# Kernel tuning notes

Measured on AMD Instinct MI355X. Metric: run time of the kernel, lower is better.

## Reference

```python
import jax, jax.numpy as jnp
import numpy as np

NU, NV, NF = 100000, 50000, 5000
D = 64
S, EUV = 5, 500000
EUF, EVF, EFU, EFV = 1000000, 500000, 1000000, 500000


def _spmm(rows, cols, vals, x, n_out):
    # COO sparse @ dense: out[r] += v * x[c]
    return jax.ops.segment_sum(vals[:, None] * x[cols], rows, num_segments=n_out)


def setup_inputs() -> dict:
    key = jax.random.key(0)
    ks = iter(jax.random.split(key, 32))
    f32 = jnp.float32
    inp = {
        'x_u': jax.random.normal(next(ks), (NU, D), f32),
        'x_v': jax.random.normal(next(ks), (NV, D), f32),
        'x_f': jax.random.normal(next(ks), (NF, D), f32),
    }
    for w in ['W_u_uv', 'W_v_uv', 'W_f2u', 'W_f2v', 'W_u2f', 'W_v2f']:
        inp[w] = jax.random.normal(next(ks), (D, D), f32) * (1.0 / np.sqrt(D))
    def edges(name, shape, n_row, n_col):
        inp[name + '_rows'] = jax.random.randint(next(ks), shape, 0, n_row, jnp.int32)
        inp[name + '_cols'] = jax.random.randint(next(ks), shape, 0, n_col, jnp.int32)
        inp[name + '_vals'] = jax.random.uniform(next(ks), shape, f32)
    edges('uv', (S, EUV), NU, NV)
    edges('vu', (S, EUV), NV, NU)
    edges('uf', (EUF,), NU, NF)
    edges('vf', (EVF,), NV, NF)
    edges('fu', (EFU,), NF, NU)
    edges('fv', (EFV,), NF, NV)
    return inp


def reference(x_u, x_v, x_f, W_u_uv, W_v_uv, W_f2u, W_f2v, W_u2f, W_v2f,
              uv_rows, uv_cols, uv_vals, vu_rows, vu_cols, vu_vals,
              uf_rows, uf_cols, uf_vals, vf_rows, vf_cols, vf_vals,
              fu_rows, fu_cols, fu_vals, fv_rows, fv_cols, fv_vals):
    nu, nv, nf = x_u.shape[0], x_v.shape[0], x_f.shape[0]
    # dense feature transforms (dropout=0 -> identity)
    u2f = x_u @ W_u2f
    v2f = x_v @ W_v2f
    f2u = x_f @ W_f2u
    f2v = x_f @ W_f2v
    tmp_u = x_u @ W_u_uv
    tmp_v = x_v @ W_v_uv
    # sum over rating supports == one segment_sum over flattened edges
    msg_u = _spmm(uv_rows.reshape(-1), uv_cols.reshape(-1), uv_vals.reshape(-1), tmp_v, nu)
    msg_v = _spmm(vu_rows.reshape(-1), vu_cols.reshape(-1), vu_vals.reshape(-1), tmp_u, nv)
    msg_u = msg_u + _spmm(uf_rows, uf_cols, uf_vals, f2u, nu)
    msg_v = msg_v + _spmm(vf_rows, vf_cols, vf_vals, f2v, nv)
    msg_f = _spmm(fu_rows, fu_cols, fu_vals, u2f, nf) + _spmm(fv_rows, fv_cols, fv_vals, v2f, nf)
    return jax.nn.relu(msg_u), jax.nn.relu(msg_v), jax.nn.relu(msg_f)
```

## Files before the change

kernel.cpp:

```cpp
#include <hip/hip_runtime.h>


#define TDIM 64
#define EPB  4096

struct Rel {
    const int* rows; const int* cols; const float* vals;
    int n, chunk0, boff, shift, srcflag, eoff, coladd;
};
struct RelPack { Rel r[6]; };

struct TPack {
    const float* X[3]; const float* W1[3]; const float* W2[3];
    unsigned short* Y1[3]; unsigned short* Y2[3];
    int N[3]; int c0[3];
};

struct FSPack {
    int c0A[3], cntA[3], offA[3];
    int c0B[3], cntB[3], offB[3];
};

struct GatherPack {
    const unsigned* srcA[3]; const unsigned* srcB[3];
    int n0, n1;
};

__device__ __forceinline__ unsigned short f2bf(float f) {
    union { float f; unsigned u; } c; c.f = f;
    unsigned r = c.u + 0x7FFFu + ((c.u >> 16) & 1u);
    return (unsigned short)(r >> 16);
}
__device__ __forceinline__ float bflo(unsigned x) { return __uint_as_float(x << 16); }
__device__ __forceinline__ float bfhi(unsigned x) { return __uint_as_float(x & 0xFFFF0000u); }
__device__ __forceinline__ float pval(unsigned p) {
    return __uint_as_float((p & 0x7FFFu) << 16);
}

__global__ __launch_bounds__(256) void transform_fused_kernel(TPack T)
{
    __shared__ float xsT[64 * 68];
    __shared__ float w1s[64 * 64];
    __shared__ float w2s[64 * 64];

    int t = 0;
    if ((int)blockIdx.x >= T.c0[1]) t = 1;
    if ((int)blockIdx.x >= T.c0[2]) t = 2;
    const float* __restrict__ X  = T.X[t];
    const float* __restrict__ W1 = T.W1[t];
    const float* __restrict__ W2 = T.W2[t];
    unsigned short* __restrict__ Y1 = T.Y1[t];
    unsigned short* __restrict__ Y2 = T.Y2[t];
    const int N    = T.N[t];
    const int row0 = (blockIdx.x - T.c0[t]) * 64;
    const int tid  = threadIdx.x;

    for (int i = tid * 4; i < 4096; i += 256 * 4) {
        *(float4*)&w1s[i] = *(const float4*)&W1[i];
        *(float4*)&w2s[i] = *(const float4*)&W2[i];
    }
    {
        const int r  = tid >> 2;
        const int c0 = (tid & 3) * 16;
        const int gr = row0 + r;
        #pragma unroll
        for (int cc = 0; cc < 16; cc += 4) {
            const int c = c0 + cc;
            float4 v = make_float4(0.f, 0.f, 0.f, 0.f);
            if (gr < N) v = *(const float4*)&X[(size_t)gr * TDIM + c];
            xsT[(c + 0) * 68 + r] = v.x;
            xsT[(c + 1) * 68 + r] = v.y;
            xsT[(c + 2) * 68 + r] = v.z;
            xsT[(c + 3) * 68 + r] = v.w;
        }
    }
    __syncthreads();

    const int tx = tid & 15;
    const int ty = tid >> 4;
    float a1[4][4] = {{0.f}}, a2[4][4] = {{0.f}};

    #pragma unroll 8
    for (int k = 0; k < 64; ++k) {
        const float4 xv = *(const float4*)&xsT[k * 68 + ty * 4];
        const float4 w1 = *(const float4*)&w1s[k * 64 + tx * 4];
        const float4 w2 = *(const float4*)&w2s[k * 64 + tx * 4];
        const float xr[4] = {xv.x, xv.y, xv.z, xv.w};
        const float c1[4] = {w1.x, w1.y, w1.z, w1.w};
        const float c2[4] = {w2.x, w2.y, w2.z, w2.w};
        #pragma unroll
        for (int r = 0; r < 4; ++r)
            #pragma unroll
            for (int c = 0; c < 4; ++c) {
                a1[r][c] = fmaf(xr[r], c1[c], a1[r][c]);
                a2[r][c] = fmaf(xr[r], c2[c], a2[r][c]);
            }
    }
    #pragma unroll
    for (int r = 0; r < 4; ++r) {
        const int gr = row0 + ty * 4 + r;
        if (gr < N) {
            ushort4 o1, o2;
            o1.x = f2bf(a1[r][0]); o1.y = f2bf(a1[r][1]);
            o1.z = f2bf(a1[r][2]); o1.w = f2bf(a1[r][3]);
            o2.x = f2bf(a2[r][0]); o2.y = f2bf(a2[r][1]);
            o2.z = f2bf(a2[r][2]); o2.w = f2bf(a2[r][3]);
            ((ushort4*)Y1)[(size_t)gr * 16 + tx] = o1;
            ((ushort4*)Y2)[(size_t)gr * 16 + tx] = o2;
        }
    }
}

__device__ __forceinline__ int find_rel(const RelPack& P, int chunk) {
    int ri = 0;
    if (chunk >= P.r[1].chunk0) ri = 1;
    if (chunk >= P.r[2].chunk0) ri = 2;
    if (chunk >= P.r[3].chunk0) ri = 3;
    if (chunk >= P.r[4].chunk0) ri = 4;
    if (chunk >= P.r[5].chunk0) ri = 5;
    return ri;
}

__global__ __launch_bounds__(512) void bucketize_cm_kernel(
    RelPack P, unsigned* __restrict__ pay, unsigned char* __restrict__ binb,
    int* __restrict__ localStart, int* __restrict__ bucketTotal, int NB)
{
    __shared__ int cnt[1280];
    __shared__ int sh[512];
    __shared__ unsigned stage_pay[EPB];
    __shared__ unsigned char stage_bin[EPB];

    const int tid   = threadIdx.x;
    const int chunk = blockIdx.x;
    for (int t = tid; t < NB; t += 512) cnt[t] = 0;
    __syncthreads();

    const int ri = find_rel(P, chunk);
    const Rel M = P.r[ri];
    const int i0    = (chunk - M.chunk0) * EPB;
    const int rbase = M.eoff + i0;
    const int count = min(EPB, M.n - i0);

    const int mask = (1 << M.shift) - 1;
    const unsigned sf = (unsigned)M.srcflag;

    int      m_[EPB / 512];
    unsigned x_[EPB / 512];
    #pragma unroll
    for (int k = 0; k < EPB / 512; ++k) {
        const int i = i0 + tid + k * 512;
        m_[k] = -1;
        if (i < M.n) {
            const int row = M.rows[i];
            const int b   = M.boff + (row >> M.shift);
            m_[k] = (b << 8) | (row & mask);
            x_[k] = (unsigned)M.cols[i] + (unsigned)M.coladd;
            atomicAdd(&cnt[b], 1);
        }
    }
    __syncthreads();

    int myv[3]; int lsum = 0;
    #pragma unroll
    for (int j = 0; j < 3; ++j) {
        const int idx = tid * 3 + j;
        myv[j] = (idx < NB) ? cnt[idx] : 0;
        lsum += myv[j];
    }
    sh[tid] = lsum;
    __syncthreads();
    for (int off = 1; off < 512; off <<= 1) {
        const int x = (tid >= off) ? sh[tid - off] : 0;
        __syncthreads();
        sh[tid] += x;
        __syncthreads();
    }
    int prefix = tid ? sh[tid - 1] : 0;
    const size_t lb = (size_t)chunk * (NB + 1);
    #pragma unroll
    for (int j = 0; j < 3; ++j) {
        const int idx = tid * 3 + j;
        if (idx < NB) {
            localStart[lb + idx] = prefix;
            if (myv[j]) atomicAdd(&bucketTotal[idx], myv[j]);
            cnt[idx] = prefix;
        } else if (idx == NB) {
            localStart[lb + NB] = prefix;
        }
        prefix += myv[j];
    }
    __syncthreads();

    #pragma unroll
    for (int k = 0; k < EPB / 512; ++k) {
        if (m_[k] >= 0) {
            const int i   = i0 + tid + k * 512;
            const int b   = m_[k] >> 8;
            const int pos = atomicAdd(&cnt[b], 1);
            stage_pay[pos] = (x_[k] << 15) | ((unsigned)f2bf(M.vals[i]) & 0x7FFFu);
            stage_bin[pos] = (unsigned char)(((m_[k] & 255) << 1) | sf);
        }
    }
    __syncthreads();

    #pragma unroll
    for (int k = 0; k < EPB / 512; ++k) {
        const int j = tid + k * 512;
        if (j < count) pay[rbase + j] = stage_pay[j];
    }
    {
        const int nfull = count >> 2;
        unsigned* bout = (unsigned*)(binb + rbase);
        const unsigned* bsrc = (const unsigned*)stage_bin;
        for (int j = tid; j < nfull; j += 512) bout[j] = bsrc[j];
        if (tid < (count & 3)) binb[rbase + nfull * 4 + tid] = stage_bin[nfull * 4 + tid];
    }
}

__global__ __launch_bounds__(256) void bscan_kernel(
    const int* __restrict__ bucketTotal, int* __restrict__ bbase, int NB)
{
    __shared__ int sh[256];
    __shared__ int carry;
    const int t = threadIdx.x;
    if (t == 0) carry = 0;
    __syncthreads();
    for (int b0 = 0; b0 < NB; b0 += 256) {
        const int idx = b0 + t;
        const int c = (idx < NB) ? bucketTotal[idx] : 0;
        sh[t] = c;
        __syncthreads();
        for (int off = 1; off < 256; off <<= 1) {
            const int x = (t >= off) ? sh[t - off] : 0;
            __syncthreads();
            sh[t] += x;
            __syncthreads();
        }
        const int cbase = carry;
        if (idx < NB) bbase[idx] = cbase + sh[t] - c;
        __syncthreads();
        if (t == 0) carry = cbase + sh[255];
        __syncthreads();
    }
    if (t == 0) bbase[NB] = carry;
}

__global__ __launch_bounds__(512) void finesort_kernel(
    const unsigned* __restrict__ pay, const unsigned char* __restrict__ binb,
    const int* __restrict__ localStart, const int* __restrict__ bbase,
    FSPack F, int* __restrict__ p2, unsigned* __restrict__ arena,
    int nbU, int nbV, int NU, int NV, int NF, int NB, int ntot_rows)
{
    __shared__ int cnt[512];
    __shared__ int sh[512];
    __shared__ int runS[1024], runE[1024];

    const int b   = blockIdx.x;
    const int tid = threadIdx.x;

    int t, lb, rowbase;
    if (b < nbU)              { t = 0; lb = b;              rowbase = 0; }
    else if (b < nbU + nbV)   { t = 1; lb = b - nbU;        rowbase = NU; }
    else                      { t = 2; lb = b - nbU - nbV;  rowbase = NU + NV; }
    const int shift     = (t == 2) ? 6 : 7;
    const int Ntype     = (t == 0) ? NU : (t == 1) ? NV : NF;
    const int row_start = lb << shift;
    const int nrows     = min(1 << shift, Ntype - row_start);
    const int nbins     = (1 << shift) * 2;
    const int grow0     = rowbase + row_start;

    const int nA = F.cntA[t], nB_ = F.cntB[t];
    const int nRuns = nA + nB_;

    for (int i = tid; i < nRuns; i += 512) {
        int c, base;
        if (i < nA) { c = F.c0A[t] + i;        base = F.offA[t] + i * EPB; }
        else        { int k = i - nA;
                      c = F.c0B[t] + k;        base = F.offB[t] + k * EPB; }
        const size_t lbi = (size_t)c * (NB + 1) + b;
        runS[i] = base + localStart[lbi];
        runE[i] = base + localStart[lbi + 1];
    }
    if (tid < nbins) cnt[tid] = 0;
    __syncthreads();

    const int s = bbase[b];
    const int e = bbase[b + 1];
    const int grp = tid >> 4;
    const int gl  = tid & 15;

    for (int ridx = grp; ridx < nRuns; ridx += 32) {
        const int rs = runS[ridx], re = runE[ridx];
        for (int j = rs + gl; j < re; j += 16) {
            atomicAdd(&cnt[binb[j]], 1);
        }
    }
    __syncthreads();

    const int v = (tid < nbins) ? cnt[tid] : 0;
    sh[tid] = v;
    __syncthreads();
    for (int off = 1; off < 512; off <<= 1) {
        const int x = (tid >= off) ? sh[tid - off] : 0;
        __syncthreads();
        sh[tid] += x;
        __syncthreads();
    }
    const int excl = sh[tid] - v;
    if (tid < nbins) cnt[tid] = excl;
    if (tid < nrows * 2) p2[2 * grow0 + tid] = s + excl;
    if (b == NB - 1 && tid == 0) p2[2 * ntot_rows] = e;
    __syncthreads();

    for (int ridx = grp; ridx < nRuns; ridx += 32) {
        const int rs = runS[ridx], re = runE[ridx];
        for (int j = rs + gl; j < re; j += 16) {
            const int bin = binb[j];
            const int pos = s + atomicAdd(&cnt[bin], 1);
            arena[pos] = pay[j];
        }
    }
}

__device__ __forceinline__ void accum_seg(
    const unsigned* __restrict__ src, const unsigned* __restrict__ arena,
    const int s, const int e, const int g, const int li4,
    float (&acc)[8])
{
    if (s >= e) return;
    const int nb = (e - s + 7) >> 3;
    const unsigned* __restrict__ srcp = src + li4;

    unsigned x0[4], x1[4], x2[4], x3[4];
    float w0, w1, w2, w3;

    auto issue = [&](int j, unsigned* x, float& w) {
        const int idx = j + g;
        const bool ok = idx < e;
        const unsigned cv = arena[ok ? idx : s];
        w = ok ? pval(cv) : 0.f;
        const uint4 xv = *(const uint4*)&srcp[(cv >> 15) * 32u];
        x[0] = xv.x; x[1] = xv.y; x[2] = xv.z; x[3] = xv.w;
    };
    auto fmab = [&](const unsigned* x, float w) {
        #pragma unroll
        for (int q = 0; q < 4; ++q) {
            acc[2 * q]     = fmaf(w, bflo(x[q]), acc[2 * q]);
            acc[2 * q + 1] = fmaf(w, bfhi(x[q]), acc[2 * q + 1]);
        }
    };

    issue(s,      x0, w0);
    issue(s + 8,  x1, w1);
    issue(s + 16, x2, w2);
    issue(s + 24, x3, w3);
    __builtin_amdgcn_sched_barrier(0);

    int k = 0;
    for (;;) {
        fmab(x0, w0);
        if (k + 4 < nb) issue(s + (k + 4) * 8, x0, w0);
        __builtin_amdgcn_sched_barrier(0);
        if (++k >= nb) break;
        fmab(x1, w1);
        if (k + 4 < nb) issue(s + (k + 4) * 8, x1, w1);
        __builtin_amdgcn_sched_barrier(0);
        if (++k >= nb) break;
        fmab(x2, w2);
        if (k + 4 < nb) issue(s + (k + 4) * 8, x2, w2);
        __builtin_amdgcn_sched_barrier(0);
        if (++k >= nb) break;
        fmab(x3, w3);
        if (k + 4 < nb) issue(s + (k + 4) * 8, x3, w3);
        __builtin_amdgcn_sched_barrier(0);
        if (++k >= nb) break;
    }
}

__global__ __launch_bounds__(256) void gather_all_kernel(
    const int* __restrict__ p2, const unsigned* __restrict__ arena,
    GatherPack G, float* __restrict__ out, int nrow_total)
{
    const int gid  = (blockIdx.x * 256 + threadIdx.x) >> 6;
    const int lane = threadIdx.x & 63;
    const int g    = lane >> 3;
    const int li   = lane & 7;
    const int li4  = li * 4;
    if (gid >= nrow_total) return;
    const int wid = nrow_total - 1 - gid;

    int seg = 0;
    if (wid >= G.n1)      seg = 2;
    else if (wid >= G.n0) seg = 1;
    seg = __builtin_amdgcn_readfirstlane(seg);

    const int pa = __builtin_amdgcn_readfirstlane(p2[2 * wid]);
    const int pe = __builtin_amdgcn_readfirstlane(p2[2 * wid + 2]);

    float acc[8];
    #pragma unroll
    for (int k = 0; k < 8; ++k) acc[k] = 0.f;

    if (seg < 2) {
        accum_seg(G.srcA[seg], arena, pa, pe, g, li4, acc);
    } else {
        const int pm = __builtin_amdgcn_readfirstlane(p2[2 * wid + 1]);
        accum_seg(G.srcA[2], arena, pa, pm, g, li4, acc);
        accum_seg(G.srcB[2], arena, pm, pe, g, li4, acc);
    }

    #pragma unroll
    for (int k = 0; k < 8; ++k) {
        acc[k] += __shfl_xor(acc[k], 8, 64);
        acc[k] += __shfl_xor(acc[k], 16, 64);
        acc[k] += __shfl_xor(acc[k], 32, 64);
    }

    if (g == 0) {
        float4 o0, o1;
        o0.x = fmaxf(acc[0], 0.f); o0.y = fmaxf(acc[1], 0.f);
        o0.z = fmaxf(acc[2], 0.f); o0.w = fmaxf(acc[3], 0.f);
        o1.x = fmaxf(acc[4], 0.f); o1.y = fmaxf(acc[5], 0.f);
        o1.z = fmaxf(acc[6], 0.f); o1.w = fmaxf(acc[7], 0.f);
        float4* dst = (float4*)(out + (size_t)wid * 64 + li * 8);
        dst[0] = o0;
        dst[1] = o1;
    }
}

extern "C" void kernel_launch(void* const* d_in, const int* in_sizes, int n_in,
                              void* d_out, int out_size, void* d_ws, size_t ws_size,
                              hipStream_t stream)
{
    const float* x_u    = (const float*)d_in[0];
    const float* x_v    = (const float*)d_in[1];
    const float* x_f    = (const float*)d_in[2];
    const float* W_u_uv = (const float*)d_in[3];
    const float* W_v_uv = (const float*)d_in[4];
    const float* W_f2u  = (const float*)d_in[5];
    const float* W_f2v  = (const float*)d_in[6];
    const float* W_u2f  = (const float*)d_in[7];
    const float* W_v2f  = (const float*)d_in[8];

    const int* rows_[6] = {(const int*)d_in[9],  (const int*)d_in[12],
                           (const int*)d_in[15], (const int*)d_in[18],
                           (const int*)d_in[21], (const int*)d_in[24]};
    const int* cols_[6] = {(const int*)d_in[10], (const int*)d_in[13],
                           (const int*)d_in[16], (const int*)d_in[19],
                           (const int*)d_in[22], (const int*)d_in[25]};
    const float* vals_[6] = {(const float*)d_in[11], (const float*)d_in[14],
                             (const float*)d_in[17], (const float*)d_in[20],
                             (const float*)d_in[23], (const float*)d_in[26]};

    const int NU = in_sizes[0] / TDIM;
    const int NV = in_sizes[1] / TDIM;
    const int NF = in_sizes[2] / TDIM;
    const int E_[6] = {in_sizes[9], in_sizes[12], in_sizes[15],
                       in_sizes[18], in_sizes[21], in_sizes[24]};

    const int nbU = (NU + 127) >> 7;
    const int nbV = (NV + 127) >> 7;
    const int nbF = (NF + 63) >> 6;
    const int NB  = nbU + nbV + nbF;
    const int ntot_rows = NU + NV + NF;

    const int boff_[6]   = {0, nbU, 0, nbU, nbU + nbV, nbU + nbV};
    const int shift_[6]  = {7, 7, 7, 7, 6, 6};
    const int sflag_[6]  = {0, 0, 1, 1, 0, 1};
    const int coladd_[6] = {0, 0, NV, NU, 0, 0};

    size_t etot = 0;
    int eoff_[6];
    for (int r = 0; r < 6; ++r) { eoff_[r] = (int)etot; etot += (size_t)E_[r]; }

    RelPack P;
    int nchunks = 0;
    int relchunks[6];
    for (int r = 0; r < 6; ++r) {
        P.r[r].rows = rows_[r]; P.r[r].cols = cols_[r]; P.r[r].vals = vals_[r];
        P.r[r].n = E_[r]; P.r[r].chunk0 = nchunks;
        P.r[r].boff = boff_[r]; P.r[r].shift = shift_[r]; P.r[r].srcflag = sflag_[r];
        P.r[r].eoff = eoff_[r]; P.r[r].coladd = coladd_[r];
        relchunks[r] = (E_[r] + EPB - 1) / EPB;
        nchunks += relchunks[r];
    }

    char* wsb = (char*)d_ws;
    size_t o = 0;
    auto alloc = [&](size_t bytes) {
        char* p = wsb + o;
        o = (o + bytes + 15) & ~(size_t)15;
        return p;
    };
    unsigned short* utab = (unsigned short*)alloc(((size_t)NV + NF) * TDIM * 2);
    unsigned short* vtab = (unsigned short*)alloc(((size_t)NU + NF) * TDIM * 2);
    unsigned short* u2f  = (unsigned short*)alloc((size_t)NU * TDIM * 2);
    unsigned short* v2f  = (unsigned short*)alloc((size_t)NV * TDIM * 2);
    unsigned short* tmp_v = utab;
    unsigned short* f2u   = utab + (size_t)NV * TDIM;
    unsigned short* tmp_u = vtab;
    unsigned short* f2v   = vtab + (size_t)NU * TDIM;
    int* localStart  = (int*)alloc((size_t)nchunks * (NB + 1) * 4);
    int* bucketTotal = (int*)alloc((size_t)NB * 4);
    int* bbase       = (int*)alloc((size_t)(NB + 1) * 4);
    int* p2          = (int*)alloc((size_t)(2 * ntot_rows + 1) * 4);
    unsigned* pay        = (unsigned*)alloc(etot * 4);
    unsigned char* binb  = (unsigned char*)alloc(etot);
    unsigned* arena      = (unsigned*)alloc(etot * 4);
    (void)ws_size;

    TPack T;
    T.X[0] = x_u; T.W1[0] = W_u_uv; T.W2[0] = W_u2f; T.Y1[0] = tmp_u; T.Y2[0] = u2f; T.N[0] = NU;
    T.X[1] = x_v; T.W1[1] = W_v_uv; T.W2[1] = W_v2f; T.Y1[1] = tmp_v; T.Y2[1] = v2f; T.N[1] = NV;
    T.X[2] = x_f; T.W1[2] = W_f2u;  T.W2[2] = W_f2v; T.Y1[2] = f2u;  T.Y2[2] = f2v; T.N[2] = NF;
    T.c0[0] = 0;
    T.c0[1] = (NU + 63) / 64;
    T.c0[2] = T.c0[1] + (NV + 63) / 64;
    const int tchunks = T.c0[2] + (NF + 63) / 64;
    transform_fused_kernel<<<tchunks, 256, 0, stream>>>(T);

    hipMemsetAsync(bucketTotal, 0, (size_t)NB * sizeof(int), stream);
    bucketize_cm_kernel<<<nchunks, 512, 0, stream>>>(P, pay, binb, localStart, bucketTotal, NB);
    bscan_kernel<<<1, 256, 0, stream>>>(bucketTotal, bbase, NB);

    FSPack F;
    const int Arel[3] = {0, 1, 4}, Brel[3] = {2, 3, 5};
    for (int t = 0; t < 3; ++t) {
        F.c0A[t] = P.r[Arel[t]].chunk0; F.cntA[t] = relchunks[Arel[t]]; F.offA[t] = eoff_[Arel[t]];
        F.c0B[t] = P.r[Brel[t]].chunk0; F.cntB[t] = relchunks[Brel[t]]; F.offB[t] = eoff_[Brel[t]];
    }
    finesort_kernel<<<NB, 512, 0, stream>>>(
        pay, binb, localStart, bbase, F, p2, arena, nbU, nbV, NU, NV, NF, NB, ntot_rows);

    GatherPack G;
    G.srcA[0] = (const unsigned*)utab;  G.srcB[0] = (const unsigned*)utab;
    G.srcA[1] = (const unsigned*)vtab;  G.srcB[1] = (const unsigned*)vtab;
    G.srcA[2] = (const unsigned*)u2f;   G.srcB[2] = (const unsigned*)v2f;
    G.n0 = NU; G.n1 = NU + NV;

    gather_all_kernel<<<(ntot_rows + 3) / 4, 256, 0, stream>>>(
        p2, arena, G, (float*)d_out, ntot_rows);
}
```

Measured before the change: 524.5 us.

## Stage finesort scatter in LDS, transpose localStart, shrink F buckets

```diff
diff --git a/kernel.cpp b/kernel.cpp
--- a/kernel.cpp
+++ b/kernel.cpp
@@ -3,6 +3,7 @@
 
 #define TDIM 64
 #define EPB  4096
+#define STCAP 10240
 
 struct Rel {
     const int* rows; const int* cols; const float* vals;
@@ -125,7 +126,7 @@
     RelPack P, unsigned* __restrict__ pay, unsigned char* __restrict__ binb,
     int* __restrict__ localStart, int* __restrict__ bucketTotal, int NB)
 {
-    __shared__ int cnt[1280];
+    __shared__ int cnt[1536];
     __shared__ int sh[512];
     __shared__ unsigned stage_pay[EPB];
     __shared__ unsigned char stage_bin[EPB];
@@ -217,6 +218,27 @@
     }
 }
 
+__global__ __launch_bounds__(256) void transpose_ls_kernel(
+    const int* __restrict__ src, int* __restrict__ dst, int rows, int cols)
+{
+    __shared__ int tile[32][33];
+    const int c0 = blockIdx.x * 32;
+    const int r0 = blockIdx.y * 32;
+    const int tx = threadIdx.x & 31;
+    const int ty = threadIdx.x >> 5;
+    #pragma unroll
+    for (int k = 0; k < 32; k += 8) {
+        const int r = r0 + ty + k, c = c0 + tx;
+        if (r < rows && c < cols) tile[ty + k][tx] = src[(size_t)r * cols + c];
+    }
+    __syncthreads();
+    #pragma unroll
+    for (int k = 0; k < 32; k += 8) {
+        const int c = c0 + ty + k, r = r0 + tx;
+        if (c < cols && r < rows) dst[(size_t)c * rows + r] = tile[tx][ty + k];
+    }
+}
+
 __global__ __launch_bounds__(256) void bscan_kernel(
     const int* __restrict__ bucketTotal, int* __restrict__ bbase, int NB)
 {
@@ -247,13 +269,15 @@
 
 __global__ __launch_bounds__(512) void finesort_kernel(
     const unsigned* __restrict__ pay, const unsigned char* __restrict__ binb,
-    const int* __restrict__ localStart, const int* __restrict__ bbase,
+    const int* __restrict__ TL, const int* __restrict__ bbase,
     FSPack F, int* __restrict__ p2, unsigned* __restrict__ arena,
-    int nbU, int nbV, int NU, int NV, int NF, int NB, int ntot_rows)
+    int nbU, int nbV, int NU, int NV, int NF, int NB, int ntot_rows,
+    int nchunksTot)
 {
     __shared__ int cnt[512];
     __shared__ int sh[512];
     __shared__ int runS[1024], runE[1024];
+    __shared__ unsigned stage[STCAP];
 
     const int b   = blockIdx.x;
     const int tid = threadIdx.x;
@@ -262,7 +286,7 @@
     if (b < nbU)              { t = 0; lb = b;              rowbase = 0; }
     else if (b < nbU + nbV)   { t = 1; lb = b - nbU;        rowbase = NU; }
     else                      { t = 2; lb = b - nbU - nbV;  rowbase = NU + NV; }
-    const int shift     = (t == 2) ? 6 : 7;
+    const int shift     = (t == 2) ? 5 : 7;
     const int Ntype     = (t == 0) ? NU : (t == 1) ? NV : NF;
     const int row_start = lb << shift;
     const int nrows     = min(1 << shift, Ntype - row_start);
@@ -272,20 +296,22 @@
     const int nA = F.cntA[t], nB_ = F.cntB[t];
     const int nRuns = nA + nB_;
 
+    const int* __restrict__ TLb  = TL + (size_t)b * nchunksTot;
+    const int* __restrict__ TLb1 = TL + (size_t)(b + 1) * nchunksTot;
     for (int i = tid; i < nRuns; i += 512) {
-        int c, base;
-        if (i < nA) { c = F.c0A[t] + i;        base = F.offA[t] + i * EPB; }
+        int ci, base;
+        if (i < nA) { ci = F.c0A[t] + i;        base = F.offA[t] + i * EPB; }
         else        { int k = i - nA;
-                      c = F.c0B[t] + k;        base = F.offB[t] + k * EPB; }
-        const size_t lbi = (size_t)c * (NB + 1) + b;
-        runS[i] = base + localStart[lbi];
-        runE[i] = base + localStart[lbi + 1];
+                      ci = F.c0B[t] + k;        base = F.offB[t] + k * EPB; }
+        runS[i] = base + TLb[ci];
+        runE[i] = base + TLb1[ci];
     }
     if (tid < nbins) cnt[tid] = 0;
     __syncthreads();
 
     const int s = bbase[b];
     const int e = bbase[b + 1];
+    const bool staged = (e - s) <= STCAP;
     const int grp = tid >> 4;
     const int gl  = tid & 15;
 
@@ -307,17 +333,29 @@
         __syncthreads();
     }
     const int excl = sh[tid] - v;
-    if (tid < nbins) cnt[tid] = excl;
+    if (tid < nbins) cnt[tid] = staged ? excl : (s + excl);
     if (tid < nrows * 2) p2[2 * grow0 + tid] = s + excl;
     if (b == NB - 1 && tid == 0) p2[2 * ntot_rows] = e;
     __syncthreads();
 
-    for (int ridx = grp; ridx < nRuns; ridx += 32) {
-        const int rs = runS[ridx], re = runE[ridx];
-        for (int j = rs + gl; j < re; j += 16) {
-            const int bin = binb[j];
-            const int pos = s + atomicAdd(&cnt[bin], 1);
-            arena[pos] = pay[j];
+    if (staged) {
+        for (int ridx = grp; ridx < nRuns; ridx += 32) {
+            const int rs = runS[ridx], re = runE[ridx];
+            for (int j = rs + gl; j < re; j += 16) {
+                const int pos = atomicAdd(&cnt[binb[j]], 1);
+                stage[pos] = pay[j];
+            }
+        }
+        __syncthreads();
+        const int seglen = e - s;
+        for (int j = tid; j < seglen; j += 512) arena[s + j] = stage[j];
+    } else {
+        for (int ridx = grp; ridx < nRuns; ridx += 32) {
+            const int rs = runS[ridx], re = runE[ridx];
+            for (int j = rs + gl; j < re; j += 16) {
+                const int pos = atomicAdd(&cnt[binb[j]], 1);
+                arena[pos] = pay[j];
+            }
         }
     }
 }
@@ -460,12 +498,12 @@
 
     const int nbU = (NU + 127) >> 7;
     const int nbV = (NV + 127) >> 7;
-    const int nbF = (NF + 63) >> 6;
+    const int nbF = (NF + 31) >> 5;
     const int NB  = nbU + nbV + nbF;
     const int ntot_rows = NU + NV + NF;
 
     const int boff_[6]   = {0, nbU, 0, nbU, nbU + nbV, nbU + nbV};
-    const int shift_[6]  = {7, 7, 7, 7, 6, 6};
+    const int shift_[6]  = {7, 7, 7, 7, 5, 5};
     const int sflag_[6]  = {0, 0, 1, 1, 0, 1};
     const int coladd_[6] = {0, 0, NV, NU, 0, 0};
 
@@ -501,6 +539,7 @@
     unsigned short* tmp_u = vtab;
     unsigned short* f2v   = vtab + (size_t)NU * TDIM;
     int* localStart  = (int*)alloc((size_t)nchunks * (NB + 1) * 4);
+    int* TL          = (int*)alloc((size_t)(NB + 1) * nchunks * 4);
     int* bucketTotal = (int*)alloc((size_t)NB * 4);
     int* bbase       = (int*)alloc((size_t)(NB + 1) * 4);
     int* p2          = (int*)alloc((size_t)(2 * ntot_rows + 1) * 4);
@@ -522,6 +561,10 @@
     hipMemsetAsync(bucketTotal, 0, (size_t)NB * sizeof(int), stream);
     bucketize_cm_kernel<<<nchunks, 512, 0, stream>>>(P, pay, binb, localStart, bucketTotal, NB);
     bscan_kernel<<<1, 256, 0, stream>>>(bucketTotal, bbase, NB);
+    {
+        dim3 tgrid((NB + 1 + 31) / 32, (nchunks + 31) / 32);
+        transpose_ls_kernel<<<tgrid, 256, 0, stream>>>(localStart, TL, nchunks, NB + 1);
+    }
 
     FSPack F;
     const int Arel[3] = {0, 1, 4}, Brel[3] = {2, 3, 5};
@@ -530,7 +573,7 @@
         F.c0B[t] = P.r[Brel[t]].chunk0; F.cntB[t] = relchunks[Brel[t]]; F.offB[t] = eoff_[Brel[t]];
     }
     finesort_kernel<<<NB, 512, 0, stream>>>(
-        pay, binb, localStart, bbase, F, p2, arena, nbU, nbV, NU, NV, NF, NB, ntot_rows);
+        pay, binb, TL, bbase, F, p2, arena, nbU, nbV, NU, NV, NF, NB, ntot_rows, nchunks);
 
     GatherPack G;
     G.srcA[0] = (const unsigned*)utab;  G.srcB[0] = (const unsigned*)utab;
```

New measurement: 512.5 us. 2.3% less time.
